# Optimization experiments

Measured on AMD Instinct MI355X. Metric: run time of the kernel, lower is better.

## Reference

```python
import jax, jax.numpy as jnp
import numpy as np
from jax import lax

# problem sizes and solver hyperparameters
B, N, G, T = 8, 128, 100, 24
N_ITERS, LR, RHO = 40, 2e-4, 10.0
VOLL, VOSP = 1000.0, 50.0
RES_UP, RES_DN, RT_UP, RT_DN, RAMP_F = 0.05, 0.02, 2.0, 0.5, 1.0


def setup_inputs() -> dict:
    k = jax.random.split(jax.random.key(0), 8)
    pmin = jax.random.uniform(k[0], (G,), minval=10.0, maxval=50.0)
    pmax = pmin + jax.random.uniform(k[1], (G,), minval=100.0, maxval=300.0)
    b_G = jax.random.uniform(k[2], (G,), minval=10.0, maxval=40.0)
    c_G = jax.random.uniform(k[3], (G,), minval=0.0, maxval=5.0)
    lo, hi = pmin.sum(), pmax.sum()
    forecast = lo + jax.random.uniform(k[4], (B, T)) * 0.5 * (hi - lo)
    omega_scen = 0.05 * hi * jax.random.normal(k[5], (B, N, T))
    om_min = omega_scen.min(axis=1) - 1.0
    om_max = omega_scen.max(axis=1) + 1.0
    eps = jax.random.uniform(k[6], (B,)) * 5.0
    return dict(forecast=forecast, omega_scen=omega_scen, om_min=om_min,
                om_max=om_max, eps=eps, pmin=pmin, pmax=pmax, b_G=b_G, c_G=c_G)


def _solve_one(forecast, omega, om_min, om_max, eps, pmin, pmax, b, c):
    # forecast [T], omega [N,T], om_min/om_max [T], eps scalar
    ramp = pmax * RAMP_F
    rup_p, rdn_p = RES_UP * b, RES_DN * b
    rtu_p, rtd_p = RT_UP * b, RT_DN * b
    dist_max = (om_max[None, :] - omega).sum(-1)   # [N]
    dist_min = (omega - om_min[None, :]).sum(-1)   # [N]

    def objective(v):
        Cost = b[:, None] * v['P'] + c[:, None]
        stage1 = (Cost.sum() + (rup_p[:, None] * v['R_up']).sum()
                  + (rdn_p[:, None] * v['R_dn']).sum())
        Qn = (jnp.einsum('g,ngt->n', rtu_p, v['d_up'])
              + jnp.einsum('g,ngt->n', rtd_p, v['d_dn'])
              + VOLL * v['LS'].sum(-1) + VOSP * v['SP'].sum(-1))
        Qmax = ((rtu_p[:, None] * v['du_max']).sum() + (rtd_p[:, None] * v['dd_max']).sum()
                + VOLL * v['LS_max'].sum() + VOSP * v['SP_max'].sum())
        Qmin = ((rtu_p[:, None] * v['du_min']).sum() + (rtd_p[:, None] * v['dd_min']).sum()
                + VOLL * v['LS_min'].sum() + VOSP * v['SP_min'].sum())
        # epigraph phi[n] >= Qn, >= Qmax - gamma*dist_max, >= Qmin - gamma*dist_min
        phi = jnp.maximum(Qn, jnp.maximum(Qmax - v['gamma'] * dist_max,
                                          Qmin - v['gamma'] * dist_min))
        obj = stage1 + phi.mean() + eps * v['gamma']
        return obj, (phi, Cost)

    def penalty(v):
        relu = jax.nn.relu
        dP = v['P'][:, 1:] - v['P'][:, :-1]
        res = [
            # equality constraints
            v['P'].sum(0) - forecast,
            (v['d_up'] - v['d_dn']).sum(1) + v['LS'] - v['SP'] - omega,
            (v['du_max'] - v['dd_max']).sum(0) + v['LS_max'] - v['SP_max'] - om_max,
            (v['du_min'] - v['dd_min']).sum(0) + v['LS_min'] - v['SP_min'] - om_min,
            # inequality constraints (relu of violation)
            relu(v['P'] + v['R_up'] - pmax[:, None]),
            relu(pmin[:, None] - (v['P'] - v['R_dn'])),
            relu(v['d_up'] - v['R_up'][None]),
            relu(v['d_dn'] - v['R_dn'][None]),
            relu(v['du_max'] - v['R_up']), relu(v['dd_max'] - v['R_dn']),
            relu(v['du_min'] - v['R_up']), relu(v['dd_min'] - v['R_dn']),
            relu(jnp.abs(dP) - ramp[:, None]),
        ]
        total = jnp.zeros(())
        for r in res:
            total = total + (r * r).sum()
        return total

    def loss(v):
        return objective(v)[0] + RHO * penalty(v)

    def project(v):
        v = {kk: jnp.maximum(vv, 0.0) for kk, vv in v.items()}
        v['P'] = jnp.clip(v['P'], pmin[:, None], pmax[:, None])
        return v

    z_gt = jnp.zeros((G, T))
    v0 = {'P': jnp.broadcast_to(0.5 * (pmin + pmax)[:, None], (G, T)),
          'R_up': z_gt, 'R_dn': z_gt,
          'd_up': jnp.zeros((N, G, T)), 'd_dn': jnp.zeros((N, G, T)),
          'LS': jnp.zeros((N, T)), 'SP': jnp.zeros((N, T)),
          'du_max': z_gt, 'dd_max': z_gt,
          'LS_max': jnp.zeros((T,)), 'SP_max': jnp.zeros((T,)),
          'du_min': z_gt, 'dd_min': z_gt,
          'LS_min': jnp.zeros((T,)), 'SP_min': jnp.zeros((T,)),
          'gamma': jnp.zeros(())}
    grad_fn = jax.grad(loss)

    def step(v, _):
        g = grad_fn(v)
        v = jax.tree_util.tree_map(lambda x, gx: x - LR * gx, v, g)
        return project(v), None

    v, _ = lax.scan(step, v0, None, length=N_ITERS)
    obj, (phi, Cost) = objective(v)
    return v['P'], v['R_up'], v['R_dn'], Cost, phi, v['gamma'], obj


def reference(forecast, omega_scen, om_min, om_max, eps, pmin, pmax, b_G, c_G):
    solve = jax.vmap(_solve_one, in_axes=(0, 0, 0, 0, 0, None, None, None, None))
    P, R_up, R_dn, Cost, phi, gamma, obj = solve(
        forecast, omega_scen, om_min, om_max, eps, pmin, pmax, b_G, c_G)
    return P, R_up, R_dn, Cost, phi, gamma, obj
```

## Files before the change

### kernel.cpp

```cpp
#include <hip/hip_runtime.h>
#include <hip/hip_cooperative_groups.h>

namespace cg = cooperative_groups;

#define G_ 100
#define T_ 24
#define NSC 128
#define BATCH 8
#define NITER 40
#define NBLK (BATCH*T_)
#define NTHR 512
#define GMAX 15

typedef unsigned long long u64;

__device__ __forceinline__ u64 gload64(const u64* p){
  return __hip_atomic_load(p, __ATOMIC_RELAXED, __HIP_MEMORY_SCOPE_AGENT);
}
__device__ __forceinline__ void gstore64(u64* p, u64 v){
  __hip_atomic_store(p, v, __ATOMIC_RELAXED, __HIP_MEMORY_SCOPE_AGENT);
}
__device__ __forceinline__ u64 pack(float v, unsigned tag){
  return ((u64)tag<<32) | (u64)__float_as_uint(v);
}
__device__ __forceinline__ float unpackv(u64 x){ return __uint_as_float((unsigned)x); }
__device__ __forceinline__ unsigned unpackt(u64 x){ return (unsigned)(x>>32); }

__device__ __forceinline__ void blockReduce2(float& a, float& b, float* sR){
#pragma unroll
  for (int off=32; off; off>>=1){ a+=__shfl_down(a,off,64); b+=__shfl_down(b,off,64); }
  const int w = threadIdx.x>>6;
  __syncthreads();
  if ((threadIdx.x&63)==0){ sR[w]=a; sR[8+w]=b; }
  __syncthreads();
  a=0.f; b=0.f;
#pragma unroll
  for (int i=0;i<8;++i){ a+=sR[i]; b+=sR[8+i]; }
}

__global__ __launch_bounds__(NTHR, 1) void dro_kernel(
    const float* __restrict__ forecast, const float* __restrict__ omega,
    const float* __restrict__ om_min, const float* __restrict__ om_max,
    const float* __restrict__ eps_in, const float* __restrict__ pmin_g,
    const float* __restrict__ pmax_g, const float* __restrict__ bG,
    const float* __restrict__ cG, float* __restrict__ out, float* __restrict__ ws)
{
  constexpr float LR=2e-4f, VOLL=1000.f, VOSP=50.f, TWO_RHO=20.f, INVN=1.f/128.f;
  const int blk=blockIdx.x;
  const int b=blk&7;
  const int t_own=blk>>3;
  const int tid=threadIdx.x, wave=tid>>6, lane=tid&63;
  int gbase, gcnt;
  if      (wave==0){ gbase=0;  gcnt=14; }
  else if (wave==1){ gbase=0;  gcnt=0;  }
  else if (wave==2){ gbase=14; gcnt=15; }
  else if (wave==3){ gbase=29; gcnt=15; }
  else             { gbase=44+(wave-4)*14; gcnt=14; }
  const bool pA = (wave!=1);

  __shared__ float sRu[2][G_], sRd[2][G_];
  __shared__ float sP[G_];
  __shared__ float sAccU[G_], sAccD[G_];
  __shared__ float sB[G_], sPmin[G_], sPmax[G_], sC[G_];
  __shared__ float sLS[NSC], sSP[NSC], sOm[NSC];
  __shared__ float sQn[NSC], sDM[NSC], sDm[NSC], sS2[NSC];
  __shared__ float sQp[NSC*9], sSp[NSC*9];
  __shared__ float sQnP[NTHR];
  __shared__ float sRed[40];
  __shared__ float sScal[8];

  u64* W = (u64*)ws;
  u64* QNP = W;
  u64* PP  = W + 73728;
  u64* QS  = W + 147456;
  u64* GAM = W + 156672;
  u64* ST1 = W + 157056;

  const float epsv  = eps_in[b];
  const float omaxT = om_max[b*T_ + t_own];
  const float ominT = om_min[b*T_ + t_own];
  const float fctT  = forecast[b*T_ + t_own];

  float duA[GMAX], duB[GMAX], ddA[GMAX], ddB[GMAX];
  float duMr[2]={0.f,0.f}, ddMr[2]={0.f,0.f}, dumr[2]={0.f,0.f}, ddmr[2]={0.f,0.f};
  float lsm=0.f, spm=0.f, lsn=0.f, spn=0.f;
  float r3reg=0.f, r4reg=0.f, rPreg=0.f;

  if (tid<G_){
    sB[tid]=bG[tid]; sPmin[tid]=pmin_g[tid]; sPmax[tid]=pmax_g[tid]; sC[tid]=cG[tid];
    sRu[0][tid]=0.f; sRd[0][tid]=0.f;
    sAccU[tid]=0.f; sAccD[tid]=0.f;
  }
  if (tid<NSC){
    const int nn=tid;
    sLS[nn]=0.f; sSP[nn]=0.f; sS2[nn]=0.f;
    sOm[nn]=omega[(b*NSC+nn)*T_+t_own];
    float dM=0.f,dm=0.f;
    for (int t=0;t<T_;++t){
      float o=omega[(b*NSC+nn)*T_+t];
      dM+=om_max[b*T_+t]-o; dm+=o-om_min[b*T_+t];
    }
    sDM[nn]=dM; sDm[nn]=dm;
    sQp[nn*9+1]=0.f; sSp[nn*9+1]=0.f;
  }
  if (tid<6) sScal[tid]=0.f;
  __syncthreads();
#pragma unroll
  for (int j=0;j<GMAX;++j){ duA[j]=0.f; duB[j]=0.f; ddA[j]=0.f; ddB[j]=0.f; }
  {
    float p0=0.f;
    if (tid<G_){
      p0=0.5f*(sPmin[tid]+sPmax[tid]);
      sP[tid]=p0;
      gstore64(&PP[b*3072 + t_own*128 + tid], pack(p0,1u));
    }
    if (tid<NSC) gstore64(&QNP[b*3072 + t_own*128 + tid], pack(0.f,1u));
    float rp=p0, dum0=0.f;
    blockReduce2(rp,dum0,sRed);
    r3reg=-omaxT; r4reg=-ominT; rPreg=rp-fctT;
  }
  __syncthreads();

  for (int k=0;k<=NITER;++k){
    const unsigned tg  = (unsigned)(k+1);
    const unsigned tg2 = (unsigned)(k+2);
    const int rb = k%3, wb = (k+1)%3;
    const int kb = k&1, nbuf = kb^1;
    const int par = k&1, parN = par^1;
    float* sRuC = sRu[kb];  float* sRdC = sRd[kb];
    float* sRuN = sRu[nbuf]; float* sRdN = sRd[nbuf];
    const u64* qnpR = QNP + rb*24576 + b*3072;
    const u64* ppR  = PP  + rb*24576 + b*3072;
    u64* qnpW = QNP + wb*24576 + b*3072 + t_own*128;
    u64* ppW  = PP  + wb*24576 + b*3072 + t_own*128;
    u64* qsW  = QS  + (wb*BATCH + b)*T_*16 + t_own*16;
    const u64* qsN = QS + (wb*BATCH + b)*T_*16;
    u64* gamW = GAM + (wb*BATCH + b)*16;
    const u64* gamN = gamW;

    const int n = tid&127, sb0 = (tid>>7)*6;
    const bool w1 = (wave==1), hasG1 = w1 && (lane<36);
    const bool doP = w1 && (k<NITER);
    u64 xq[6];
#pragma unroll
    for (int s=0;s<6;++s) xq[s]=gload64(&qnpR[(sb0+s)*128+n]);
    u64 xm0=0,xm1=0,xp0=0,xp1=0;
    if (doP){
      if (t_own>0){
        xm0=gload64(&ppR[(t_own-1)*128+lane]);
        if (hasG1) xm1=gload64(&ppR[(t_own-1)*128+lane+64]);
      }
      if (t_own<T_-1){
        xp0=gload64(&ppR[(t_own+1)*128+lane]);
        if (hasG1) xp1=gload64(&ppR[(t_own+1)*128+lane+64]);
      }
    }
    for (;;){
      bool pend=false;
#pragma unroll
      for (int s=0;s<6;++s)
        if (unpackt(xq[s])!=tg){ xq[s]=gload64(&qnpR[(sb0+s)*128+n]); pend=true; }
      if (doP){
        if (t_own>0){
          if (unpackt(xm0)!=tg){ xm0=gload64(&ppR[(t_own-1)*128+lane]); pend=true; }
          if (hasG1 && unpackt(xm1)!=tg){ xm1=gload64(&ppR[(t_own-1)*128+lane+64]); pend=true; }
        }
        if (t_own<T_-1){
          if (unpackt(xp0)!=tg){ xp0=gload64(&ppR[(t_own+1)*128+lane]); pend=true; }
          if (hasG1 && unpackt(xp1)!=tg){ xp1=gload64(&ppR[(t_own+1)*128+lane+64]); pend=true; }
        }
      }
      if (!pend) break;
      __builtin_amdgcn_s_sleep(1);
    }
    sQnP[tid]=unpackv(xq[0])+unpackv(xq[1])+unpackv(xq[2])
             +unpackv(xq[3])+unpackv(xq[4])+unpackv(xq[5]);
    __syncthreads();

    if (k==NITER){
      const float Qm=sScal[par*3], Qn2=sScal[par*3+1], gam=sScal[par*3+2];
      if (tid<NSC){
        const float qsum=sQnP[tid]+sQnP[tid+128]+sQnP[tid+256]+sQnP[tid+384];
        const float ph=fmaxf(qsum,fmaxf(Qm-gam*sDM[tid],Qn2-gam*sDm[tid]));
        sQn[tid]=ph;
        if (t_own==0) out[76800 + b*NSC + tid]=ph;
      }
      float st=0.f, dum0=0.f;
      if (tid<G_){
        const int g=tid;
        const float Pv=sP[g];
        const float costv=sB[g]*Pv+sC[g];
        st=costv + 0.05f*sB[g]*sRuC[g] + 0.02f*sB[g]*sRdC[g];
        const int o=b*2400 + g*T_ + t_own;
        out[o]=Pv;
        out[19200+o]=sRuC[g];
        out[38400+o]=sRdC[g];
        out[57600+o]=costv;
      }
      blockReduce2(st,dum0,sRed);
      if (tid==0) gstore64(&ST1[(b*T_+t_own)*16], pack(st,99u));
      if (t_own==0){
        if (tid==0) out[77824+b]=gam;
        float s1=0.f;
        if (tid<64){
          u64 xs = (lane<T_)? gload64(&ST1[(b*T_+lane)*16]) : pack(0.f,99u);
          while (unpackt(xs)!=99u){ __builtin_amdgcn_s_sleep(1); xs=gload64(&ST1[(b*T_+lane)*16]); }
          s1=unpackv(xs);
        }
        float pm=(tid<NSC)? sQn[tid] : 0.f;
        blockReduce2(pm,s1,sRed);
        if (tid==0) out[77832+b] = s1 + pm*INVN + epsv*gam;
      }
      break;
    }

    const float QmaxS=sScal[par*3], QminS=sScal[par*3+1], gammaS=sScal[par*3+2];
    float lsR0=0.f, lsR1=0.f, spR0=0.f, spR1=0.f;
    if (pA){
      float gqA=0.f,r220A=0.f,gqB=0.f,r220B=0.f;
#pragma unroll
      for (int h=0;h<2;++h){
        const int nn=lane+h*64;
        const float Qn=sQnP[nn]+sQnP[nn+128]+sQnP[nn+256]+sQnP[nn+384];
        const float m1=QmaxS-gammaS*sDM[nn], m2=QminS-gammaS*sDm[nn];
        const float inner=fmaxf(m1,m2), ph=fmaxf(Qn,inner);
        const float gQn=(Qn==ph?1.f:0.f)/((inner==ph)?2.f:1.f);
        const float gq=gQn*INVN;
        const float r2=sS2[nn]+sLS[nn]-sSP[nn]-sOm[nn];
        const float r220=TWO_RHO*r2;
        if (h==0){ gqA=gq; r220A=r220; } else { gqB=gq; r220B=r220; }
      }
      float qvA=0.f,qvB=0.f,svA=0.f,svB=0.f;
#pragma unroll
      for (int j=0;j<GMAX;++j){
        if (j<gcnt){
          const int g=gbase+j;
          const float bg=sB[g];
          const float rtu=2.f*bg, rtd=0.5f*bg;
          const float ru=sRuC[g], rd=sRdC[g];
          const float r7A=fmaxf(duA[j]-ru,0.f), r8A=fmaxf(ddA[j]-rd,0.f);
          const float r7B=fmaxf(duB[j]-ru,0.f), r8B=fmaxf(ddB[j]-rd,0.f);
          duA[j]=fmaxf(duA[j]-LR*(gqA*rtu+(r220A+TWO_RHO*r7A)),0.f);
          ddA[j]=fmaxf(ddA[j]-LR*(gqA*rtd+(TWO_RHO*r8A-r220A)),0.f);
          duB[j]=fmaxf(duB[j]-LR*(gqB*rtu+(r220B+TWO_RHO*r7B)),0.f);
          ddB[j]=fmaxf(ddB[j]-LR*(gqB*rtd+(TWO_RHO*r8B-r220B)),0.f);
          qvA+=rtu*duA[j]+rtd*ddA[j];  svA+=duA[j]-ddA[j];
          qvB+=rtu*duB[j]+rtd*ddB[j];  svB+=duB[j]-ddB[j];
        }
      }
      sQp[lane*9+wave]=qvA;      sSp[lane*9+wave]=svA;
      sQp[(lane+64)*9+wave]=qvB; sSp[(lane+64)*9+wave]=svB;
    } else {
      float g1l=0.f,g2l=0.f,sgl=0.f;
#pragma unroll
      for (int h=0;h<2;++h){
        const int nn=lane+h*64;
        const float Qn=sQnP[nn]+sQnP[nn+128]+sQnP[nn+256]+sQnP[nn+384];
        const float m1=QmaxS-gammaS*sDM[nn], m2=QminS-gammaS*sDm[nn];
        const float inner=fmaxf(m1,m2), ph=fmaxf(Qn,inner);
        const float gQn=(Qn==ph?1.f:0.f)/((inner==ph)?2.f:1.f);
        const float gIn=(inner==ph?1.f:0.f)/((Qn==ph)?2.f:1.f);
        const float gm1=gIn*(m1==inner?1.f:0.f)/((m2==inner)?2.f:1.f);
        const float gm2=gIn*(m2==inner?1.f:0.f)/((m1==inner)?2.f:1.f);
        const float gq=gQn*INVN;
        g1l+=gm1; g2l+=gm2; sgl+=gm1*sDM[nn]+gm2*sDm[nn];
        const float r2=sS2[nn]+sLS[nn]-sSP[nn]-sOm[nn];
        const float r220=TWO_RHO*r2;
        const float lsnew=fmaxf(sLS[nn]-LR*(gq*VOLL+r220),0.f);
        const float spnew=fmaxf(sSP[nn]-LR*(gq*VOSP-r220),0.f);
        if (h==0){ lsR0=lsnew; spR0=spnew; } else { lsR1=lsnew; spR1=spnew; }
      }
#pragma unroll
      for (int off=32; off; off>>=1){
        g1l+=__shfl_xor(g1l,off,64); g2l+=__shfl_xor(g2l,off,64); sgl+=__shfl_xor(sgl,off,64);
      }
      const float S1s=g1l, S2s=g2l;
      if (t_own==0 && lane==0)
        gstore64(gamW, pack(fmaxf(gammaS-LR*(epsv-INVN*sgl),0.f), tg2));
      const float r3=__shfl(r3reg,0,64), r4=__shfl(r4reg,0,64), rP=__shfl(rPreg,0,64);
      float pQx=0.f,pQn2=0.f,pr3=0.f,pr4=0.f,pP=0.f;
#pragma unroll
      for (int i=0;i<2;++i){
        if (i==0 || hasG1){
          const int g = lane + i*64;
          const float rupS=sAccU[g], rdnS=sAccD[g];
          const float Pold=sP[g], ru=sRuC[g], rd=sRdC[g];
          const float duMo=duMr[i], ddMo=ddMr[i], dumo=dumr[i], ddmo=ddmr[i];
          const float r5 =fmaxf(Pold+ru-sPmax[g],0.f);
          const float r6 =fmaxf(sPmin[g]-Pold+rd,0.f);
          const float r9 =fmaxf(duMo-ru,0.f), r10=fmaxf(ddMo-rd,0.f);
          const float r11=fmaxf(dumo-ru,0.f), r12=fmaxf(ddmo-rd,0.f);
          const float rampg=sPmax[g];
          float gP=sB[g]+TWO_RHO*(rP+r5-r6);
          if (t_own>0){
            const float dp=Pold-unpackv(i==0?xm0:xm1);
            gP+=TWO_RHO*fmaxf(fabsf(dp)-rampg,0.f)*(dp>=0.f?1.f:-1.f);
          }
          if (t_own<T_-1){
            const float dq=unpackv(i==0?xp0:xp1)-Pold;
            gP-=TWO_RHO*fmaxf(fabsf(dq)-rampg,0.f)*(dq>=0.f?1.f:-1.f);
          }
          const float Pn=fminf(fmaxf(Pold-LR*gP,sPmin[g]),sPmax[g]);
          sP[g]=Pn; gstore64(&ppW[g], pack(Pn,tg2));
          const float rtuB=2.f*sB[g], rtdB=0.5f*sB[g];
          sRuN[g]=fmaxf(ru-LR*(0.05f*sB[g]+TWO_RHO*(r5-rupS-r9-r11)),0.f);
          sRdN[g]=fmaxf(rd-LR*(0.02f*sB[g]+TWO_RHO*(r6-rdnS-r10-r12)),0.f);
          const float duMn=fmaxf(duMo-LR*(INVN*S1s*rtuB+TWO_RHO*( r3+r9 )),0.f);
          const float ddMn=fmaxf(ddMo-LR*(INVN*S1s*rtdB+TWO_RHO*(-r3+r10)),0.f);
          const float dumn=fmaxf(dumo-LR*(INVN*S2s*rtuB+TWO_RHO*( r4+r11)),0.f);
          const float ddmn=fmaxf(ddmo-LR*(INVN*S2s*rtdB+TWO_RHO*(-r4+r12)),0.f);
          duMr[i]=duMn; ddMr[i]=ddMn; dumr[i]=dumn; ddmr[i]=ddmn;
          pQx+=rtuB*duMn+rtdB*ddMn; pQn2+=rtuB*dumn+rtdB*ddmn;
          pr3+=duMn-ddMn; pr4+=dumn-ddmn; pP+=Pn;
        }
      }
#pragma unroll
      for (int off=32; off; off>>=1){
        pQx+=__shfl_down(pQx,off,64);  pQn2+=__shfl_down(pQn2,off,64);
        pr3+=__shfl_down(pr3,off,64);  pr4+=__shfl_down(pr4,off,64);
        pP +=__shfl_down(pP,off,64);
      }
      if (lane==0){
        const float LSMn=fmaxf(lsm-LR*(INVN*S1s*VOLL+TWO_RHO*r3),0.f);
        const float SPMn=fmaxf(spm-LR*(INVN*S1s*VOSP-TWO_RHO*r3),0.f);
        const float LSmn=fmaxf(lsn-LR*(INVN*S2s*VOLL+TWO_RHO*r4),0.f);
        const float SPmn=fmaxf(spn-LR*(INVN*S2s*VOSP-TWO_RHO*r4),0.f);
        lsm=LSMn; spm=SPMn; lsn=LSmn; spn=SPmn;
        gstore64(&qsW[0], pack(pQx + VOLL*LSMn + VOSP*SPMn, tg2));
        gstore64(&qsW[1], pack(pQn2 + VOLL*LSmn + VOSP*SPmn, tg2));
        r3reg=pr3 + LSMn - SPMn - omaxT;
        r4reg=pr4 + LSmn - SPmn - ominT;
        rPreg=pP - fctT;
      }
    }
    __syncthreads();

    if (pA){
#pragma unroll
      for (int j=0;j<GMAX;++j){
        if (j<gcnt){
          const int g=gbase+j;
          const float ru=sRuN[g], rd=sRdN[g];
          float aU=fmaxf(duA[j]-ru,0.f)+fmaxf(duB[j]-ru,0.f);
          float aD=fmaxf(ddA[j]-rd,0.f)+fmaxf(ddB[j]-rd,0.f);
#pragma unroll
          for (int off=32; off; off>>=1){ aU+=__shfl_xor(aU,off,64); aD+=__shfl_xor(aD,off,64); }
          if (lane==0){ sAccU[g]=aU; sAccD[g]=aD; }
        }
      }
    } else {
      u64 yq0=0, yq1=0, yg;
      if (lane<T_){ yq0=gload64(&qsN[lane*16]); yq1=gload64(&qsN[lane*16+1]); }
      yg=gload64(gamN);
#pragma unroll
      for (int h=0;h<2;++h){
        const int nn=lane+h*64;
        const float LSn=(h==0?lsR0:lsR1), SPn=(h==0?spR0:spR1);
        sLS[nn]=LSn; sSP[nn]=SPn;
        float q=0.f,s=0.f;
#pragma unroll
        for (int w=0;w<8;++w){ q+=sQp[nn*9+w]; s+=sSp[nn*9+w]; }
        sS2[nn]=s;
        q += VOLL*LSn + VOSP*SPn;
        gstore64(&qnpW[nn], pack(q,tg2));
      }
      for (;;){
        bool pend=false;
        if (lane<T_){
          if (unpackt(yq0)!=tg2){ yq0=gload64(&qsN[lane*16]);   pend=true; }
          if (unpackt(yq1)!=tg2){ yq1=gload64(&qsN[lane*16+1]); pend=true; }
        }
        if (unpackt(yg)!=tg2){ yg=gload64(gamN); pend=true; }
        if (!pend) break;
        __builtin_amdgcn_s_sleep(1);
      }
      float qmx=(lane<T_)?unpackv(yq0):0.f, qmn=(lane<T_)?unpackv(yq1):0.f;
#pragma unroll
      for (int off=32; off; off>>=1){ qmx+=__shfl_xor(qmx,off,64); qmn+=__shfl_xor(qmn,off,64); }
      if (lane==0){ sScal[parN*3]=qmx; sScal[parN*3+1]=qmn; sScal[parN*3+2]=unpackv(yg); }
    }
  }
}

extern "C" void kernel_launch(void* const* d_in, const int* in_sizes, int n_in,
                              void* d_out, int out_size, void* d_ws, size_t ws_size,
                              hipStream_t stream) {
  const float* forecast = (const float*)d_in[0];
  const float* omega    = (const float*)d_in[1];
  const float* omin     = (const float*)d_in[2];
  const float* omax     = (const float*)d_in[3];
  const float* eps      = (const float*)d_in[4];
  const float* pmin     = (const float*)d_in[5];
  const float* pmax     = (const float*)d_in[6];
  const float* bG       = (const float*)d_in[7];
  const float* cG       = (const float*)d_in[8];
  float* out = (float*)d_out;
  float* ws  = (float*)d_ws;
  void* args[] = { &forecast, &omega, &omin, &omax, &eps, &pmin, &pmax, &bG, &cG, &out, &ws };
  hipLaunchCooperativeKernel((const void*)dro_kernel, dim3(NBLK), dim3(NTHR),
                             args, 0, stream);
}
```

Before: 408.1 us.

## Poll per-block ready flags instead of spinning on all tagged data words

Each block now publishes a per-iteration ready flag in a spare slot of the QS array after writing its QNP/PP data. Consumers poll only a few flag words per wave until they are ready, then read the tagged data, instead of spinning on every data word. The data loads for the next iteration are issued early, at the end of the previous iteration, so a wait is needed only when a tag is stale. This cuts the polling traffic on the inter-block exchange. In exchange it adds an extra store and an s_waitcnt before signalling, and correctness now rests on the ordering between the data stores and the flag store.

```diff
diff --git a/kernel.cpp b/kernel.cpp
--- a/kernel.cpp
+++ b/kernel.cpp
@@ -120,6 +120,26 @@
     r3reg=-omaxT; r4reg=-ominT; rPreg=rp-fctT;
   }
   __syncthreads();
+  if (tid==0) gstore64(&QS[b*T_*16 + t_own*16 + 8], pack(0.f,1u));
+
+  u64 xq[6]; u64 xm0=0,xm1=0,xp0=0,xp1=0;
+  {
+    const int n0 = tid&127, sb00 = (tid>>7)*6;
+    const u64* qnp0 = QNP + b*3072;
+#pragma unroll
+    for (int s=0;s<6;++s) xq[s]=gload64(&qnp0[(sb00+s)*128+n0]);
+    if (wave==1){
+      const u64* pp0 = PP + b*3072;
+      if (t_own>0){
+        xm0=gload64(&pp0[(t_own-1)*128+lane]);
+        if (lane<36) xm1=gload64(&pp0[(t_own-1)*128+lane+64]);
+      }
+      if (t_own<T_-1){
+        xp0=gload64(&pp0[(t_own+1)*128+lane]);
+        if (lane<36) xp1=gload64(&pp0[(t_own+1)*128+lane+64]);
+      }
+    }
+  }
 
   for (int k=0;k<=NITER;++k){
     const unsigned tg  = (unsigned)(k+1);
@@ -131,6 +151,7 @@
     float* sRuN = sRu[nbuf]; float* sRdN = sRd[nbuf];
     const u64* qnpR = QNP + rb*24576 + b*3072;
     const u64* ppR  = PP  + rb*24576 + b*3072;
+    const u64* flagR= QS  + (rb*BATCH + b)*T_*16;
     u64* qnpW = QNP + wb*24576 + b*3072 + t_own*128;
     u64* ppW  = PP  + wb*24576 + b*3072 + t_own*128;
     u64* qsW  = QS  + (wb*BATCH + b)*T_*16 + t_own*16;
@@ -141,37 +162,44 @@
     const int n = tid&127, sb0 = (tid>>7)*6;
     const bool w1 = (wave==1), hasG1 = w1 && (lane<36);
     const bool doP = w1 && (k<NITER);
-    u64 xq[6];
-#pragma unroll
-    for (int s=0;s<6;++s) xq[s]=gload64(&qnpR[(sb0+s)*128+n]);
-    u64 xm0=0,xm1=0,xp0=0,xp1=0;
-    if (doP){
-      if (t_own>0){
-        xm0=gload64(&ppR[(t_own-1)*128+lane]);
-        if (hasG1) xm1=gload64(&ppR[(t_own-1)*128+lane+64]);
-      }
-      if (t_own<T_-1){
-        xp0=gload64(&ppR[(t_own+1)*128+lane]);
-        if (hasG1) xp1=gload64(&ppR[(t_own+1)*128+lane+64]);
-      }
-    }
-    for (;;){
+    {
       bool pend=false;
 #pragma unroll
-      for (int s=0;s<6;++s)
-        if (unpackt(xq[s])!=tg){ xq[s]=gload64(&qnpR[(sb0+s)*128+n]); pend=true; }
+      for (int s=0;s<6;++s) pend |= (unpackt(xq[s])!=tg);
       if (doP){
-        if (t_own>0){
-          if (unpackt(xm0)!=tg){ xm0=gload64(&ppR[(t_own-1)*128+lane]); pend=true; }
-          if (hasG1 && unpackt(xm1)!=tg){ xm1=gload64(&ppR[(t_own-1)*128+lane+64]); pend=true; }
-        }
-        if (t_own<T_-1){
-          if (unpackt(xp0)!=tg){ xp0=gload64(&ppR[(t_own+1)*128+lane]); pend=true; }
-          if (hasG1 && unpackt(xp1)!=tg){ xp1=gload64(&ppR[(t_own+1)*128+lane+64]); pend=true; }
-        }
-      }
-      if (!pend) break;
-      __builtin_amdgcn_s_sleep(1);
+        if (t_own>0){ pend |= (unpackt(xm0)!=tg); if (hasG1) pend |= (unpackt(xm1)!=tg); }
+        if (t_own<T_-1){ pend |= (unpackt(xp0)!=tg); if (hasG1) pend |= (unpackt(xp1)!=tg); }
+      }
+      if (__any(pend)){
+        int ft=-1;
+        if (lane<6) ft=sb0+lane;
+        else if (doP && lane==6 && t_own>0)     ft=t_own-1;
+        else if (doP && lane==7 && t_own<T_-1)  ft=t_own+1;
+        for (;;){
+          bool fok=true;
+          if (ft>=0) fok = (unpackt(gload64(&flagR[ft*16+8]))==tg);
+          if (__all(fok)) break;
+          __builtin_amdgcn_s_sleep(1);
+        }
+        asm volatile("" ::: "memory");
+        for (;;){
+          bool p2=false;
+#pragma unroll
+          for (int s=0;s<6;++s)
+            if (unpackt(xq[s])!=tg){ xq[s]=gload64(&qnpR[(sb0+s)*128+n]); p2=true; }
+          if (doP){
+            if (t_own>0){
+              if (unpackt(xm0)!=tg){ xm0=gload64(&ppR[(t_own-1)*128+lane]); p2=true; }
+              if (hasG1 && unpackt(xm1)!=tg){ xm1=gload64(&ppR[(t_own-1)*128+lane+64]); p2=true; }
+            }
+            if (t_own<T_-1){
+              if (unpackt(xp0)!=tg){ xp0=gload64(&ppR[(t_own+1)*128+lane]); p2=true; }
+              if (hasG1 && unpackt(xp1)!=tg){ xp1=gload64(&ppR[(t_own+1)*128+lane+64]); p2=true; }
+            }
+          }
+          if (!p2) break;
+        }
+      }
     }
     sQnP[tid]=unpackv(xq[0])+unpackv(xq[1])+unpackv(xq[2])
              +unpackv(xq[3])+unpackv(xq[4])+unpackv(xq[5]);
@@ -336,6 +364,9 @@
     __syncthreads();
 
     if (pA){
+      const u64* qnpN = QNP + wb*24576 + b*3072;
+#pragma unroll
+      for (int s=0;s<6;++s) xq[s]=gload64(&qnpN[(sb0+s)*128+n]);
 #pragma unroll
       for (int j=0;j<GMAX;++j){
         if (j<gcnt){
@@ -349,9 +380,6 @@
         }
       }
     } else {
-      u64 yq0=0, yq1=0, yg;
-      if (lane<T_){ yq0=gload64(&qsN[lane*16]); yq1=gload64(&qsN[lane*16+1]); }
-      yg=gload64(gamN);
 #pragma unroll
       for (int h=0;h<2;++h){
         const int nn=lane+h*64;
@@ -364,6 +392,26 @@
         q += VOLL*LSn + VOSP*SPn;
         gstore64(&qnpW[nn], pack(q,tg2));
       }
+      asm volatile("" ::: "memory");
+      __builtin_amdgcn_s_waitcnt(0);
+      if (lane==0) gstore64(&qsW[8], pack(0.f,tg2));
+      const u64* qnpN = QNP + wb*24576 + b*3072;
+#pragma unroll
+      for (int s=0;s<6;++s) xq[s]=gload64(&qnpN[(sb0+s)*128+n]);
+      if (k+1<NITER){
+        const u64* ppN = PP + wb*24576 + b*3072;
+        if (t_own>0){
+          xm0=gload64(&ppN[(t_own-1)*128+lane]);
+          if (lane<36) xm1=gload64(&ppN[(t_own-1)*128+lane+64]);
+        }
+        if (t_own<T_-1){
+          xp0=gload64(&ppN[(t_own+1)*128+lane]);
+          if (lane<36) xp1=gload64(&ppN[(t_own+1)*128+lane+64]);
+        }
+      }
+      u64 yq0=0, yq1=0, yg;
+      if (lane<T_){ yq0=gload64(&qsN[lane*16]); yq1=gload64(&qsN[lane*16+1]); }
+      yg=gload64(gamN);
       for (;;){
         bool pend=false;
         if (lane<T_){
```

Measured after the change: 520.6 us. 27.6% more time.

## Speculatively precompute scenario updates for all three gradient cases off the critical path

Applied to the files above, without the earlier changes.

The per-scenario d_up/d_dn update depends on a subgradient weight gQn that can only be 0, 0.5 or 1, so the kernel now precomputes the resulting partial sums for all three cases in the previous iteration's tail, after the barrier, and just selects the matching one once gQn is known. The actual state update moves to after the barrier as well. Wave 0 takes over the LS/SP update and the cross-wave reduction that publishes QNP, using a shared-memory counter in place of a block barrier. This is meant to shorten the latency-critical path between the global exchanges, at the cost of roughly triple the arithmetic in the slack phase and an extra spin-wait. It also relies on gQn being exactly one of the three values.

```diff
diff --git a/kernel.cpp b/kernel.cpp
--- a/kernel.cpp
+++ b/kernel.cpp
@@ -46,6 +46,7 @@
     const float* __restrict__ cG, float* __restrict__ out, float* __restrict__ ws)
 {
   constexpr float LR=2e-4f, VOLL=1000.f, VOSP=50.f, TWO_RHO=20.f, INVN=1.f/128.f;
+  constexpr float GQ1=0.5f*INVN, GQ2=1.0f*INVN;
   const int blk=blockIdx.x;
   const int b=blk&7;
   const int t_own=blk>>3;
@@ -68,6 +69,7 @@
   __shared__ float sQnP[NTHR];
   __shared__ float sRed[40];
   __shared__ float sScal[8];
+  __shared__ unsigned sCnt[2];
 
   u64* W = (u64*)ws;
   u64* QNP = W;
@@ -82,6 +84,10 @@
   const float fctT  = forecast[b*T_ + t_own];
 
   float duA[GMAX], duB[GMAX], ddA[GMAX], ddB[GMAX];
+  float qvA0=0.f,qvA1=0.f,qvA2=0.f, svA0=0.f,svA1=0.f,svA2=0.f;
+  float qvB0=0.f,qvB1=0.f,qvB2=0.f, svB0=0.f,svB1=0.f,svB2=0.f;
+  float gQnA=0.f, gQnB=0.f;
+  float r220Ac=0.f, r220Bc=0.f;
   float duMr[2]={0.f,0.f}, ddMr[2]={0.f,0.f}, dumr[2]={0.f,0.f}, ddmr[2]={0.f,0.f};
   float lsm=0.f, spm=0.f, lsn=0.f, spn=0.f;
   float r3reg=0.f, r4reg=0.f, rPreg=0.f;
@@ -104,6 +110,7 @@
     sQp[nn*9+1]=0.f; sSp[nn*9+1]=0.f;
   }
   if (tid<6) sScal[tid]=0.f;
+  if (tid==0){ sCnt[0]=0u; sCnt[1]=0u; }
   __syncthreads();
 #pragma unroll
   for (int j=0;j<GMAX;++j){ duA[j]=0.f; duB[j]=0.f; ddA[j]=0.f; ddB[j]=0.f; }
@@ -120,6 +127,40 @@
     r3reg=-omaxT; r4reg=-ominT; rPreg=rp-fctT;
   }
   __syncthreads();
+  if (pA){
+    const float r2A = sS2[lane]+sLS[lane]-sSP[lane]-sOm[lane];
+    const float r2B = sS2[lane+64]+sLS[lane+64]-sSP[lane+64]-sOm[lane+64];
+    r220Ac = TWO_RHO*r2A; r220Bc = TWO_RHO*r2B;
+#pragma unroll
+    for (int j=0;j<GMAX;++j){
+      if (j<gcnt){
+        const int g=gbase+j;
+        const float bg=sB[g];
+        const float rtu=2.f*bg, rtd=0.5f*bg;
+        const float ru=sRu[0][g], rd=sRd[0][g];
+        const float m7A=fmaxf(duA[j]-ru,0.f), m8A=fmaxf(ddA[j]-rd,0.f);
+        const float m7B=fmaxf(duB[j]-ru,0.f), m8B=fmaxf(ddB[j]-rd,0.f);
+        const float du0A=fmaxf(duA[j]-LR*(0.f*rtu+(r220Ac+TWO_RHO*m7A)),0.f);
+        const float dd0A=fmaxf(ddA[j]-LR*(0.f*rtd+(TWO_RHO*m8A-r220Ac)),0.f);
+        const float du1A=fmaxf(duA[j]-LR*(GQ1*rtu+(r220Ac+TWO_RHO*m7A)),0.f);
+        const float dd1A=fmaxf(ddA[j]-LR*(GQ1*rtd+(TWO_RHO*m8A-r220Ac)),0.f);
+        const float du2A=fmaxf(duA[j]-LR*(GQ2*rtu+(r220Ac+TWO_RHO*m7A)),0.f);
+        const float dd2A=fmaxf(ddA[j]-LR*(GQ2*rtd+(TWO_RHO*m8A-r220Ac)),0.f);
+        qvA0+=rtu*du0A+rtd*dd0A; svA0+=du0A-dd0A;
+        qvA1+=rtu*du1A+rtd*dd1A; svA1+=du1A-dd1A;
+        qvA2+=rtu*du2A+rtd*dd2A; svA2+=du2A-dd2A;
+        const float du0B=fmaxf(duB[j]-LR*(0.f*rtu+(r220Bc+TWO_RHO*m7B)),0.f);
+        const float dd0B=fmaxf(ddB[j]-LR*(0.f*rtd+(TWO_RHO*m8B-r220Bc)),0.f);
+        const float du1B=fmaxf(duB[j]-LR*(GQ1*rtu+(r220Bc+TWO_RHO*m7B)),0.f);
+        const float dd1B=fmaxf(ddB[j]-LR*(GQ1*rtd+(TWO_RHO*m8B-r220Bc)),0.f);
+        const float du2B=fmaxf(duB[j]-LR*(GQ2*rtu+(r220Bc+TWO_RHO*m7B)),0.f);
+        const float dd2B=fmaxf(ddB[j]-LR*(GQ2*rtd+(TWO_RHO*m8B-r220Bc)),0.f);
+        qvB0+=rtu*du0B+rtd*dd0B; svB0+=du0B-dd0B;
+        qvB1+=rtu*du1B+rtd*dd1B; svB1+=du1B-dd1B;
+        qvB2+=rtu*du2B+rtd*dd2B; svB2+=du2B-dd2B;
+      }
+    }
+  }
 
   for (int k=0;k<=NITER;++k){
     const unsigned tg  = (unsigned)(k+1);
@@ -215,9 +256,8 @@
     }
 
     const float QmaxS=sScal[par*3], QminS=sScal[par*3+1], gammaS=sScal[par*3+2];
-    float lsR0=0.f, lsR1=0.f, spR0=0.f, spR1=0.f;
     if (pA){
-      float gqA=0.f,r220A=0.f,gqB=0.f,r220B=0.f;
+      float lsnA=0.f,spnA=0.f,lsnB=0.f,spnB=0.f;
 #pragma unroll
       for (int h=0;h<2;++h){
         const int nn=lane+h*64;
@@ -225,31 +265,43 @@
         const float m1=QmaxS-gammaS*sDM[nn], m2=QminS-gammaS*sDm[nn];
         const float inner=fmaxf(m1,m2), ph=fmaxf(Qn,inner);
         const float gQn=(Qn==ph?1.f:0.f)/((inner==ph)?2.f:1.f);
-        const float gq=gQn*INVN;
-        const float r2=sS2[nn]+sLS[nn]-sSP[nn]-sOm[nn];
-        const float r220=TWO_RHO*r2;
-        if (h==0){ gqA=gq; r220A=r220; } else { gqB=gq; r220B=r220; }
-      }
-      float qvA=0.f,qvB=0.f,svA=0.f,svB=0.f;
-#pragma unroll
-      for (int j=0;j<GMAX;++j){
-        if (j<gcnt){
-          const int g=gbase+j;
-          const float bg=sB[g];
-          const float rtu=2.f*bg, rtd=0.5f*bg;
-          const float ru=sRuC[g], rd=sRdC[g];
-          const float r7A=fmaxf(duA[j]-ru,0.f), r8A=fmaxf(ddA[j]-rd,0.f);
-          const float r7B=fmaxf(duB[j]-ru,0.f), r8B=fmaxf(ddB[j]-rd,0.f);
-          duA[j]=fmaxf(duA[j]-LR*(gqA*rtu+(r220A+TWO_RHO*r7A)),0.f);
-          ddA[j]=fmaxf(ddA[j]-LR*(gqA*rtd+(TWO_RHO*r8A-r220A)),0.f);
-          duB[j]=fmaxf(duB[j]-LR*(gqB*rtu+(r220B+TWO_RHO*r7B)),0.f);
-          ddB[j]=fmaxf(ddB[j]-LR*(gqB*rtd+(TWO_RHO*r8B-r220B)),0.f);
-          qvA+=rtu*duA[j]+rtd*ddA[j];  svA+=duA[j]-ddA[j];
-          qvB+=rtu*duB[j]+rtd*ddB[j];  svB+=duB[j]-ddB[j];
-        }
-      }
+        if (h==0) gQnA=gQn; else gQnB=gQn;
+        if (wave==0){
+          const float gq=gQn*INVN;
+          const float r2=sS2[nn]+sLS[nn]-sSP[nn]-sOm[nn];
+          const float r220=TWO_RHO*r2;
+          const float lsnew=fmaxf(sLS[nn]-LR*(gq*VOLL+r220),0.f);
+          const float spnew=fmaxf(sSP[nn]-LR*(gq*VOSP-r220),0.f);
+          sLS[nn]=lsnew; sSP[nn]=spnew;
+          if (h==0){ lsnA=lsnew; spnA=spnew; } else { lsnB=lsnew; spnB=spnew; }
+        }
+      }
+      const float qvA = (gQnA==0.f)? qvA0 : ((gQnA==0.5f)? qvA1 : qvA2);
+      const float svA = (gQnA==0.f)? svA0 : ((gQnA==0.5f)? svA1 : svA2);
+      const float qvB = (gQnB==0.f)? qvB0 : ((gQnB==0.5f)? qvB1 : qvB2);
+      const float svB = (gQnB==0.f)? svB0 : ((gQnB==0.5f)? svB1 : svB2);
       sQp[lane*9+wave]=qvA;      sSp[lane*9+wave]=svA;
       sQp[(lane+64)*9+wave]=qvB; sSp[(lane+64)*9+wave]=svB;
+      __threadfence_block();
+      if (wave!=0){
+        if (lane==0)
+          __hip_atomic_fetch_add(&sCnt[par],1u,__ATOMIC_RELEASE,__HIP_MEMORY_SCOPE_WORKGROUP);
+      } else {
+        while (__hip_atomic_load(&sCnt[par],__ATOMIC_ACQUIRE,__HIP_MEMORY_SCOPE_WORKGROUP)!=6u)
+          __builtin_amdgcn_s_sleep(1);
+        __threadfence_block();
+#pragma unroll
+        for (int h=0;h<2;++h){
+          const int nn=lane+h*64;
+          float q=0.f,s=0.f;
+#pragma unroll
+          for (int w=0;w<8;++w){ q+=sQp[nn*9+w]; s+=sSp[nn*9+w]; }
+          sS2[nn]=s;
+          q += VOLL*(h?lsnB:lsnA) + VOSP*(h?spnB:spnA);
+          gstore64(&qnpW[nn], pack(q,tg2));
+        }
+        if (lane==0) sCnt[par]=0u;
+      }
     } else {
       float g1l=0.f,g2l=0.f,sgl=0.f;
 #pragma unroll
@@ -262,13 +314,8 @@
         const float gIn=(inner==ph?1.f:0.f)/((Qn==ph)?2.f:1.f);
         const float gm1=gIn*(m1==inner?1.f:0.f)/((m2==inner)?2.f:1.f);
         const float gm2=gIn*(m2==inner?1.f:0.f)/((m1==inner)?2.f:1.f);
-        const float gq=gQn*INVN;
         g1l+=gm1; g2l+=gm2; sgl+=gm1*sDM[nn]+gm2*sDm[nn];
-        const float r2=sS2[nn]+sLS[nn]-sSP[nn]-sOm[nn];
-        const float r220=TWO_RHO*r2;
-        const float lsnew=fmaxf(sLS[nn]-LR*(gq*VOLL+r220),0.f);
-        const float spnew=fmaxf(sSP[nn]-LR*(gq*VOSP-r220),0.f);
-        if (h==0){ lsR0=lsnew; spR0=spnew; } else { lsR1=lsnew; spR1=spnew; }
+        (void)gQn;
       }
 #pragma unroll
       for (int off=32; off; off>>=1){
@@ -336,34 +383,58 @@
     __syncthreads();
 
     if (pA){
+      const float gqA=gQnA*INVN, gqB=gQnB*INVN;
+      const float r2An = sS2[lane]+sLS[lane]-sSP[lane]-sOm[lane];
+      const float r2Bn = sS2[lane+64]+sLS[lane+64]-sSP[lane+64]-sOm[lane+64];
+      const float r220An=TWO_RHO*r2An, r220Bn=TWO_RHO*r2Bn;
+      qvA0=0.f;qvA1=0.f;qvA2=0.f; svA0=0.f;svA1=0.f;svA2=0.f;
+      qvB0=0.f;qvB1=0.f;qvB2=0.f; svB0=0.f;svB1=0.f;svB2=0.f;
 #pragma unroll
       for (int j=0;j<GMAX;++j){
         if (j<gcnt){
           const int g=gbase+j;
-          const float ru=sRuN[g], rd=sRdN[g];
-          float aU=fmaxf(duA[j]-ru,0.f)+fmaxf(duB[j]-ru,0.f);
-          float aD=fmaxf(ddA[j]-rd,0.f)+fmaxf(ddB[j]-rd,0.f);
+          const float bg=sB[g];
+          const float rtu=2.f*bg, rtd=0.5f*bg;
+          const float ruC=sRuC[g], rdC=sRdC[g];
+          const float r7A=fmaxf(duA[j]-ruC,0.f), r8A=fmaxf(ddA[j]-rdC,0.f);
+          const float r7B=fmaxf(duB[j]-ruC,0.f), r8B=fmaxf(ddB[j]-rdC,0.f);
+          duA[j]=fmaxf(duA[j]-LR*(gqA*rtu+(r220Ac+TWO_RHO*r7A)),0.f);
+          ddA[j]=fmaxf(ddA[j]-LR*(gqA*rtd+(TWO_RHO*r8A-r220Ac)),0.f);
+          duB[j]=fmaxf(duB[j]-LR*(gqB*rtu+(r220Bc+TWO_RHO*r7B)),0.f);
+          ddB[j]=fmaxf(ddB[j]-LR*(gqB*rtd+(TWO_RHO*r8B-r220Bc)),0.f);
+          const float ruN=sRuN[g], rdN=sRdN[g];
+          const float m7A=fmaxf(duA[j]-ruN,0.f), m7B=fmaxf(duB[j]-ruN,0.f);
+          const float m8A=fmaxf(ddA[j]-rdN,0.f), m8B=fmaxf(ddB[j]-rdN,0.f);
+          float aU=m7A+m7B;
+          float aD=m8A+m8B;
 #pragma unroll
           for (int off=32; off; off>>=1){ aU+=__shfl_xor(aU,off,64); aD+=__shfl_xor(aD,off,64); }
           if (lane==0){ sAccU[g]=aU; sAccD[g]=aD; }
-        }
-      }
+          const float du0A=fmaxf(duA[j]-LR*(0.f*rtu+(r220An+TWO_RHO*m7A)),0.f);
+          const float dd0A=fmaxf(ddA[j]-LR*(0.f*rtd+(TWO_RHO*m8A-r220An)),0.f);
+          const float du1A=fmaxf(duA[j]-LR*(GQ1*rtu+(r220An+TWO_RHO*m7A)),0.f);
+          const float dd1A=fmaxf(ddA[j]-LR*(GQ1*rtd+(TWO_RHO*m8A-r220An)),0.f);
+          const float du2A=fmaxf(duA[j]-LR*(GQ2*rtu+(r220An+TWO_RHO*m7A)),0.f);
+          const float dd2A=fmaxf(ddA[j]-LR*(GQ2*rtd+(TWO_RHO*m8A-r220An)),0.f);
+          qvA0+=rtu*du0A+rtd*dd0A; svA0+=du0A-dd0A;
+          qvA1+=rtu*du1A+rtd*dd1A; svA1+=du1A-dd1A;
+          qvA2+=rtu*du2A+rtd*dd2A; svA2+=du2A-dd2A;
+          const float du0B=fmaxf(duB[j]-LR*(0.f*rtu+(r220Bn+TWO_RHO*m7B)),0.f);
+          const float dd0B=fmaxf(ddB[j]-LR*(0.f*rtd+(TWO_RHO*m8B-r220Bn)),0.f);
+          const float du1B=fmaxf(duB[j]-LR*(GQ1*rtu+(r220Bn+TWO_RHO*m7B)),0.f);
+          const float dd1B=fmaxf(ddB[j]-LR*(GQ1*rtd+(TWO_RHO*m8B-r220Bn)),0.f);
+          const float du2B=fmaxf(duB[j]-LR*(GQ2*rtu+(r220Bn+TWO_RHO*m7B)),0.f);
+          const float dd2B=fmaxf(ddB[j]-LR*(GQ2*rtd+(TWO_RHO*m8B-r220Bn)),0.f);
+          qvB0+=rtu*du0B+rtd*dd0B; svB0+=du0B-dd0B;
+          qvB1+=rtu*du1B+rtd*dd1B; svB1+=du1B-dd1B;
+          qvB2+=rtu*du2B+rtd*dd2B; svB2+=du2B-dd2B;
+        }
+      }
+      r220Ac=r220An; r220Bc=r220Bn;
     } else {
       u64 yq0=0, yq1=0, yg;
       if (lane<T_){ yq0=gload64(&qsN[lane*16]); yq1=gload64(&qsN[lane*16+1]); }
       yg=gload64(gamN);
-#pragma unroll
-      for (int h=0;h<2;++h){
-        const int nn=lane+h*64;
-        const float LSn=(h==0?lsR0:lsR1), SPn=(h==0?spR0:spR1);
-        sLS[nn]=LSn; sSP[nn]=SPn;
-        float q=0.f,s=0.f;
-#pragma unroll
-        for (int w=0;w<8;++w){ q+=sQp[nn*9+w]; s+=sSp[nn*9+w]; }
-        sS2[nn]=s;
-        q += VOLL*LSn + VOSP*SPn;
-        gstore64(&qnpW[nn], pack(q,tg2));
-      }
       for (;;){
         bool pend=false;
         if (lane<T_){
```

New measurement: 617.4 us. +51.3%, slower.
